# Kernel optimization log

Measured on AMD Instinct MI355X. Metric: run time of the kernel, lower is better.

Reference implementation:

```python
import jax, jax.numpy as jnp
import numpy as np

B, S, D = 4, 2048, 768
H = 12
DH = D // H
NUM_WAY = 4
DFF = 4 * D  # FFN expansion scale=4
EPS = 1e-6


def setup_inputs() -> dict:
    key = jax.random.key(0)
    ks = jax.random.split(key, 20)
    s = 0.02
    inp = {
        "x": jax.random.normal(ks[0], (B, S, D), jnp.float32),
        "w": jax.random.randint(ks[1], (B, S), 0, NUM_WAY, jnp.int64),
        # LayerNorm 1
        "ln1_g": jnp.ones((D,), jnp.float32),
        "ln1_b": jnp.zeros((D,), jnp.float32),
        # Multi-head attention projections (input_dim=out_dim=D)
        "wq": jax.random.normal(ks[2], (D, D), jnp.float32) * s,
        "bq": jnp.zeros((D,), jnp.float32),
        "wk": jax.random.normal(ks[3], (D, D), jnp.float32) * s,
        "bk": jnp.zeros((D,), jnp.float32),
        "wv": jax.random.normal(ks[4], (D, D), jnp.float32) * s,
        "bv": jnp.zeros((D,), jnp.float32),
        "wo": jax.random.normal(ks[5], (D, D), jnp.float32) * s,
        "bo": jnp.zeros((D,), jnp.float32),
        # Way classifier
        "wcls": jax.random.normal(ks[6], (D, NUM_WAY), jnp.float32) * s,
        "bcls": jnp.zeros((NUM_WAY,), jnp.float32),
        # num_way stacked FFN experts: Linear(D,4D) -> ReLU -> Linear(4D,D)
        "w1": jax.random.normal(ks[7], (NUM_WAY, D, DFF), jnp.float32) * s,
        "b1": jnp.zeros((NUM_WAY, DFF), jnp.float32),
        "w2": jax.random.normal(ks[8], (NUM_WAY, DFF, D), jnp.float32) * s,
        "b2": jnp.zeros((NUM_WAY, D), jnp.float32),
    }
    return inp


def _layernorm(x, g, b):
    mu = jnp.mean(x, axis=-1, keepdims=True)
    var = jnp.mean(jnp.square(x - mu), axis=-1, keepdims=True)
    return (x - mu) * jax.lax.rsqrt(var + EPS) * g + b


def reference(x, w, ln1_g, ln1_b, wq, bq, wk, bk, wv, bv, wo, bo,
              wcls, bcls, w1, b1, w2, b2):
    # pre-LN
    xn = _layernorm(x, ln1_g, ln1_b)
    # multi-head self-attention (q = k = v = xn)
    q = (xn @ wq + bq).reshape(B, S, H, DH)
    k = (xn @ wk + bk).reshape(B, S, H, DH)
    v = (xn @ wv + bv).reshape(B, S, H, DH)
    scores = jnp.einsum('bqhd,bkhd->bhqk', q, k) / jnp.sqrt(jnp.float32(DH))
    attn = jax.nn.softmax(scores, axis=-1)
    ctx = jnp.einsum('bhqk,bkhd->bqhd', attn, v).reshape(B, S, D)
    ctx = ctx @ wo + bo
    # dropout is identity at inference; residual
    out = ctx + x
    # dense compute-all-experts FFN, then per-token select by routing id w
    # (mask-overwrite in original == one-hot select since masks partition)
    ffn_out = jnp.zeros_like(out)
    for ci in range(NUM_WAY):
        h = jax.nn.relu(out @ w1[ci] + b1[ci])        # [B,S,4D]
        fi = h @ w2[ci] + b2[ci]                      # [B,S,D]
        mask = (w == ci).astype(out.dtype)[..., None]  # [B,S,1]
        if ci == 0:
            # original initializes ffn_out with way-0 output everywhere;
            # later ways overwrite where w == ci, net = select expert w
            ffn_out = fi
        else:
            ffn_out = ffn_out * (1.0 - mask) + fi * mask
    way_logits = out @ wcls + bcls  # [B,S,NUM_WAY]
    return ffn_out, way_logits
```

## Files before the change

### kernel.cpp

```cpp
#include <hip/hip_runtime.h>
#include <cstdint>

typedef unsigned short u16;
typedef float f32x4 __attribute__((ext_vector_type(4)));
typedef float f32x16 __attribute__((ext_vector_type(16)));
typedef __bf16 bf16x8 __attribute__((ext_vector_type(8)));

#define LOG2E 1.44269504088896340736f

__device__ __forceinline__ u16 f2bf(float f) {
    union { float f; unsigned u; } v; v.f = f;
    unsigned r = v.u + 0x7fffu + ((v.u >> 16) & 1u);
    return (u16)(r >> 16);
}

__device__ __forceinline__ unsigned cvt_pk_bf16(float lo, float hi) {
    unsigned r;
    asm("v_cvt_pk_bf16_f32 %0, %1, %2" : "=v"(r) : "v"(lo), "v"(hi));
    return r;
}

__device__ __forceinline__ float exp2_hw(float x) {
    float r;
    asm("v_exp_f32 %0, %1" : "=v"(r) : "v"(x));
    return r;
}

__device__ __forceinline__ f32x4 mfma16(bf16x8 a, bf16x8 b, f32x4 c) {
    return __builtin_amdgcn_mfma_f32_16x16x32_bf16(a, b, c, 0, 0, 0);
}

__device__ __forceinline__ f32x16 mfma32(bf16x8 a, bf16x8 b, f32x16 c) {
    return __builtin_amdgcn_mfma_f32_32x32x16_bf16(a, b, c, 0, 0, 0);
}

__device__ __forceinline__ void gload_lds16(const void* g, void* l) {
    __builtin_amdgcn_global_load_lds(
        (__attribute__((address_space(1))) unsigned int*)(g),
        (__attribute__((address_space(3))) unsigned int*)(l),
        16, 0, 0);
}

#define MB_TOK 8192
#define DM 768
#define HH 12
#define DHD 64
#define NWAY 4
#define DFF 3072
#define SEQ 2048
#define NBATCH 4

__global__ __launch_bounds__(256) void ln_kernel(
    const float* __restrict__ x, const float* __restrict__ g,
    const float* __restrict__ bb, u16* __restrict__ xn)
{
    int row = blockIdx.x, t = threadIdx.x;
    const float* xr = x + (size_t)row * DM;
    float v0 = xr[t], v1 = xr[t + 256], v2 = xr[t + 512];
    float s = v0 + v1 + v2;
    __shared__ float red[4];
    #pragma unroll
    for (int k = 1; k < 64; k <<= 1) s += __shfl_xor(s, k);
    if ((t & 63) == 0) red[t >> 6] = s;
    __syncthreads();
    float mu = (red[0] + red[1] + red[2] + red[3]) * (1.f / 768.f);
    float d0 = v0 - mu, d1 = v1 - mu, d2 = v2 - mu;
    float q = d0 * d0 + d1 * d1 + d2 * d2;
    #pragma unroll
    for (int k = 1; k < 64; k <<= 1) q += __shfl_xor(q, k);
    __syncthreads();
    if ((t & 63) == 0) red[t >> 6] = q;
    __syncthreads();
    float var = (red[0] + red[1] + red[2] + red[3]) * (1.f / 768.f);
    float rs = rsqrtf(var + 1e-6f);
    u16* xo = xn + (size_t)row * DM;
    xo[t]       = f2bf(d0 * rs * g[t]       + bb[t]);
    xo[t + 256] = f2bf(d1 * rs * g[t + 256] + bb[t + 256]);
    xo[t + 512] = f2bf(d2 * rs * g[t + 512] + bb[t + 512]);
}

__global__ __launch_bounds__(256) void transpose_bf16(
    const float* __restrict__ src, u16* __restrict__ dst, int K, int N)
{
    __shared__ float tl[32][33];
    size_t bofs = (size_t)blockIdx.z * K * N;
    src += bofs; dst += bofs;
    int n0 = blockIdx.x * 32, k0 = blockIdx.y * 32;
    int tx = threadIdx.x, ty = threadIdx.y;
    #pragma unroll
    for (int j = 0; j < 4; ++j)
        tl[ty + j * 8][tx] = src[(size_t)(k0 + ty + j * 8) * N + n0 + tx];
    __syncthreads();
    #pragma unroll
    for (int j = 0; j < 4; ++j)
        dst[(size_t)(n0 + ty + j * 8) * K + k0 + tx] = f2bf(tl[tx][ty + j * 8]);
}

__global__ __launch_bounds__(256) void vT_kernel(
    const u16* __restrict__ qkv, u16* __restrict__ vT)
{
    __shared__ u16 tl[32][33];
    int bh = blockIdx.z;
    int b = bh / HH, h = bh % HH;
    int key0 = blockIdx.x * 32;
    int d0 = blockIdx.y * 32;
    int tx = threadIdx.x, ty = threadIdx.y;
    const u16* src = qkv + ((size_t)b * SEQ + key0) * 2304 + 1536 + h * 64 + d0;
    #pragma unroll
    for (int j = 0; j < 4; ++j)
        tl[ty + j * 8][tx] = src[(size_t)(ty + j * 8) * 2304 + tx];
    __syncthreads();
    u16* dst = vT + ((size_t)bh * 64 + d0) * SEQ + key0;
    #pragma unroll
    for (int j = 0; j < 4; ++j)
        dst[(size_t)(ty + j * 8) * SEQ + tx] = tl[tx][ty + j * 8];
}

__global__ void concat_bias_kernel(const float* bq, const float* bk,
                                   const float* bv, float* bqkv)
{
    int i = blockIdx.x * 256 + threadIdx.x;
    if (i < 2304) bqkv[i] = i < 768 ? bq[i] : (i < 1536 ? bk[i - 768] : bv[i - 1536]);
}

__global__ void route_kernel(const int* __restrict__ wl,
                             int* __restrict__ perm, int* __restrict__ eoff,
                             int4* __restrict__ fmap)
{
    __shared__ int cnt[4], cur[4], off[5];
    int tid = threadIdx.x;
    if (tid < 4) cnt[tid] = 0;
    __syncthreads();
    for (int t = tid; t < MB_TOK; t += 256) atomicAdd(&cnt[wl[t] & 3], 1);
    __syncthreads();
    if (tid == 0) {
        off[0] = 0;
        for (int e = 0; e < 4; ++e) off[e + 1] = off[e] + cnt[e];
        int idx = 0;
        for (int e = 0; e < 4; ++e)
            for (int s = 0; s < cnt[e]; s += 128)
                fmap[idx++] = make_int4(e, off[e], s, cnt[e] - s);
        for (; idx < 72; ++idx) fmap[idx] = make_int4(-1, 0, 0, 0);
        for (int e = 0; e < 5; ++e) eoff[e] = off[e];
        for (int e = 0; e < 4; ++e) cur[e] = off[e];
    }
    __syncthreads();
    for (int t = tid; t < MB_TOK; t += 256) {
        int e = wl[t] & 3;
        int pos = atomicAdd(&cur[e], 1);
        perm[pos] = t;
    }
}

template<int MODE, bool RELU, bool RES, bool ST32, bool ST16>
__global__ __launch_bounds__(256, 3) void gemm_bt_kernel(
    const u16* __restrict__ A, const u16* __restrict__ Bt,
    const float* __restrict__ bias, const float* __restrict__ res,
    float* __restrict__ out32, u16* __restrict__ out16,
    int nbt, int N, int K, int ntn,
    const int* __restrict__ perm, const int4* __restrict__ fmap)
{
    __shared__ __attribute__((aligned(16))) u16 As[2][4096];
    __shared__ __attribute__((aligned(16))) u16 Bs[2][4096];
    int tid = threadIdx.x;
    int wv = tid >> 6, ln = tid & 63;
    int bpx = gridDim.x / (ntn << 3);
    int jj = blockIdx.x >> 3;
    int bt = (blockIdx.x & 7) * bpx + jj / ntn;
    int tn = (jj % ntn) * 128;
    if (bt >= nbt) return;

    int seg = 0, ms = 0, mb = 128, tm = 0;
    if (MODE != 0) {
        int4 ent = fmap[bt];
        if (ent.x < 0) return;
        seg = ent.y; ms = ent.z; mb = ent.w; if (mb > 128) mb = 128;
        Bt += (size_t)ent.x * N * K;
        bias += ent.x * N;
    } else {
        tm = bt * 128;
    }

    f32x4 acc[4][4];
    #pragma unroll
    for (int i = 0; i < 4; ++i)
        #pragma unroll
        for (int j = 0; j < 4; ++j) acc[i][j] = f32x4{0.f, 0.f, 0.f, 0.f};

    int wr = wv >> 1, wc = wv & 1;
    int lr = ln & 15, hi = ln >> 4;
    int nk = K / 32;

    const u16* asrc[2];
    const u16* bsrc[2];
    #pragma unroll
    for (int i = 0; i < 2; ++i) {
        int r = (wv * 2 + i) * 16 + (ln >> 2);
        int am = r < mb ? r : (mb - 1);
        size_t arow;
        if (MODE == 1)      arow = (size_t)perm[seg + ms + am];
        else if (MODE == 2) arow = (size_t)(seg + ms + am);
        else                arow = (size_t)(tm + r);
        asrc[i] = A + arow * K + (ln & 3) * 8;
        bsrc[i] = Bt + (size_t)(tn + r) * K + (ln & 3) * 8;
    }

#define GSTAGE(bf_, k0_) do {                                             \
    gload_lds16(asrc[0] + (k0_), &As[bf_][(wv * 2) * 512]);               \
    gload_lds16(asrc[1] + (k0_), &As[bf_][(wv * 2 + 1) * 512]);           \
    gload_lds16(bsrc[0] + (k0_), &Bs[bf_][(wv * 2) * 512]);               \
    gload_lds16(bsrc[1] + (k0_), &Bs[bf_][(wv * 2 + 1) * 512]);           \
} while (0)

    GSTAGE(0, 0);
    for (int kk = 0; kk < nk; ++kk) {
        int bf = kk & 1;
        __syncthreads();
        if (kk + 1 < nk) GSTAGE(bf ^ 1, (kk + 1) * 32);
        bf16x8 a[4], b[4];
        #pragma unroll
        for (int m = 0; m < 4; ++m)
            a[m] = *(const bf16x8*)&As[bf][(wr * 64 + m * 16 + lr) * 32 + hi * 8];
        #pragma unroll
        for (int n = 0; n < 4; ++n)
            b[n] = *(const bf16x8*)&Bs[bf][(wc * 64 + n * 16 + lr) * 32 + hi * 8];
        #pragma unroll
        for (int m = 0; m < 4; ++m)
            #pragma unroll
            for (int n = 0; n < 4; ++n)
                acc[m][n] = mfma16(a[m], b[n], acc[m][n]);
    }
#undef GSTAGE

    #pragma unroll
    for (int m = 0; m < 4; ++m) {
        int rb = wr * 64 + m * 16 + hi * 4;
        #pragma unroll
        for (int n = 0; n < 4; ++n) {
            int gcol = tn + wc * 64 + n * 16 + lr;
            float bvv = bias[gcol];
            #pragma unroll
            for (int i = 0; i < 4; ++i) {
                int rml = rb + i;
                float v = acc[m][n][i] + bvv;
                if (RELU) v = v > 0.f ? v : 0.f;
                if (MODE == 0) {
                    size_t grow = (size_t)(tm + rml);
                    if (RES) v += res[grow * N + gcol];
                    if (ST32) out32[grow * N + gcol] = v;
                    if (ST16) out16[grow * N + gcol] = f2bf(v);
                } else {
                    if (rml < mb) {
                        size_t orow = (MODE == 1) ? (size_t)(seg + ms + rml)
                                                  : (size_t)perm[seg + ms + rml];
                        if (ST32) out32[orow * N + gcol] = v;
                        if (ST16) out16[orow * N + gcol] = f2bf(v);
                    }
                }
            }
        }
    }
}

__global__ __launch_bounds__(256, 4) void attn_kernel(
    const u16* __restrict__ qkv, const u16* __restrict__ vT,
    u16* __restrict__ ctx)
{
    __shared__ __attribute__((aligned(16))) u16 Ks[2][4096];
    __shared__ __attribute__((aligned(16))) u16 Vs[2][4096];
    int tid = threadIdx.x;
    int wv = tid >> 6, ln = tid & 63;
    int qv = ln & 31, hi = ln >> 5;
    int bid = blockIdx.x;
    int bh = (bid & 7) * 6 + ((bid >> 3) % 6);
    int qt = (bid >> 3) / 6;
    int b = bh / HH, h = bh % HH;
    int q0 = qt * 128 + wv * 32;
    size_t qrowb = (size_t)(b * SEQ + q0);
    const float C = 0.125f * LOG2E;

    bf16x8 qf[4];
    {
        const u16* qp = qkv + (qrowb + qv) * 2304 + h * 64 + hi * 8;
        #pragma unroll
        for (int ds = 0; ds < 4; ++ds) qf[ds] = *(const bf16x8*)(qp + ds * 16);
    }

    int csrc = 8 * ((ln & 7) ^ (ln >> 3));
    const size_t kbase = (size_t)b * SEQ * 2304 + 768 + h * 64;
    const u16* vtb = vT + (size_t)bh * 64 * SEQ;
    const u16* kp0 = qkv + kbase + (size_t)(wv * 16 + (ln >> 3)) * 2304 + csrc;
    const u16* kp1 = kp0 + (size_t)8 * 2304;
    const u16* vp0 = vtb + (size_t)(wv * 16 + (ln >> 3)) * SEQ + csrc;
    const u16* vp1 = vp0 + (size_t)8 * SEQ;

#define ATTN_STAGE(bf_, t_) do {                                          \
    gload_lds16(kp0 + (size_t)(t_) * 64 * 2304, &Ks[bf_][(wv * 2) * 512]);\
    gload_lds16(kp1 + (size_t)(t_) * 64 * 2304, &Ks[bf_][(wv * 2 + 1) * 512]);\
    gload_lds16(vp0 + (size_t)(t_) * 64, &Vs[bf_][(wv * 2) * 512]);       \
    gload_lds16(vp1 + (size_t)(t_) * 64, &Vs[bf_][(wv * 2 + 1) * 512]);   \
} while (0)

    f32x16 oacc[2];
    #pragma unroll
    for (int i = 0; i < 2; ++i)
        #pragma unroll
        for (int r = 0; r < 16; ++r) oacc[i][r] = 0.f;
    float m_run = -INFINITY, l_run = 0.f;
    int ksw = (qv & 7) * 8;

    ATTN_STAGE(0, 0);

    for (int kt = 0; kt < SEQ / 64; ++kt) {
        int bf = kt & 1;
        __syncthreads();
        if (kt + 1 < SEQ / 64) ATTN_STAGE(bf ^ 1, kt + 1);

        f32x16 s0, s1;
        #pragma unroll
        for (int r = 0; r < 16; ++r) { s0[r] = 0.f; s1[r] = 0.f; }
        #pragma unroll
        for (int ds = 0; ds < 4; ++ds) {
            bf16x8 ka0 = *(const bf16x8*)&Ks[bf][qv * 64 + ((ds * 16 + hi * 8) ^ ksw)];
            bf16x8 ka1 = *(const bf16x8*)&Ks[bf][(32 + qv) * 64 + ((ds * 16 + hi * 8) ^ ksw)];
            s0 = mfma32(ka0, qf[ds], s0);
            s1 = mfma32(ka1, qf[ds], s1);
        }

        float tmax = s0[0];
        #pragma unroll
        for (int r = 1; r < 16; ++r) tmax = fmaxf(tmax, s0[r]);
        #pragma unroll
        for (int r = 0; r < 16; ++r) tmax = fmaxf(tmax, s1[r]);
        tmax = fmaxf(tmax, __shfl_xor(tmax, 32));

        if (!__all(tmax - m_run <= 64.f)) {
            float m_new = fmaxf(m_run, tmax);
            float corr = exp2_hw((m_run - m_new) * C);
            l_run *= corr;
            #pragma unroll
            for (int i = 0; i < 2; ++i)
                #pragma unroll
                for (int r = 0; r < 16; ++r) oacc[i][r] *= corr;
            m_run = m_new;
        }
        float c2 = -m_run * C;
        float psum = 0.f;
        #pragma unroll
        for (int r = 0; r < 16; ++r) {
            s0[r] = exp2_hw(fmaf(s0[r], C, c2)); psum += s0[r];
            s1[r] = exp2_hw(fmaf(s1[r], C, c2)); psum += s1[r];
        }
        l_run += psum;

        #pragma unroll
        for (int kb = 0; kb < 2; ++kb) {
            #pragma unroll
            for (int hc = 0; hc < 2; ++hc) {
                const f32x16& sv = kb ? s1 : s0;
                unsigned x0 = cvt_pk_bf16(sv[8 * hc + 0], sv[8 * hc + 1]);
                unsigned x1 = cvt_pk_bf16(sv[8 * hc + 2], sv[8 * hc + 3]);
                unsigned x2 = cvt_pk_bf16(sv[8 * hc + 4], sv[8 * hc + 5]);
                unsigned x3 = cvt_pk_bf16(sv[8 * hc + 6], sv[8 * hc + 7]);
                unsigned t0 = hi ? x0 : x2, t1 = hi ? x1 : x3;
                unsigned r0 = (unsigned)__shfl_xor((int)t0, 32);
                unsigned r1 = (unsigned)__shfl_xor((int)t1, 32);
                union { bf16x8 v; unsigned u[4]; } pf;
                pf.u[0] = hi ? r0 : x0; pf.u[1] = hi ? r1 : x1;
                pf.u[2] = hi ? x2 : r0; pf.u[3] = hi ? x3 : r1;
                int kc = (kb * 32 + hc * 16 + hi * 8) ^ ksw;
                #pragma unroll
                for (int dblk = 0; dblk < 2; ++dblk) {
                    bf16x8 va = *(const bf16x8*)&Vs[bf][(dblk * 32 + qv) * 64 + kc];
                    oacc[dblk] = mfma32(va, pf.v, oacc[dblk]);
                }
            }
        }
    }
#undef ATTN_STAGE

    float l_tot = l_run + __shfl_xor(l_run, 32);
    float inv = 1.f / l_tot;

    __syncthreads();
    u16* eb = &Ks[0][0] + wv * 2048;
    #pragma unroll
    for (int dblk = 0; dblk < 2; ++dblk)
        #pragma unroll
        for (int r = 0; r < 16; r += 2) {
            int d = dblk * 32 + (r & 3) + 8 * (r >> 2) + 4 * hi;
            unsigned pk = cvt_pk_bf16(oacc[dblk][r] * inv, oacc[dblk][r + 1] * inv);
            *(unsigned*)&eb[qv * 64 + (d ^ ((qv & 7) * 8))] = pk;
        }
    __syncthreads();
    {
        u16* ctr = ctx + (qrowb + qv) * DM + h * 64 + hi * 32;
        #pragma unroll
        for (int g = 0; g < 4; ++g) {
            bf16x8 vv = *(const bf16x8*)&eb[qv * 64 + ((hi * 32 + g * 8) ^ ((qv & 7) * 8))];
            *(bf16x8*)(ctr + g * 8) = vv;
        }
    }
}

__global__ __launch_bounds__(256) void cls_kernel(
    const float* __restrict__ outm, const float* __restrict__ wcls,
    const float* __restrict__ bcls, float* __restrict__ dst)
{
    int row = blockIdx.x, t = threadIdx.x;
    const float* xr = outm + (size_t)row * DM;
    float a0 = 0, a1 = 0, a2 = 0, a3 = 0;
    for (int j = t; j < DM; j += 256) {
        float xv = xr[j];
        float4 wv4 = *(const float4*)(const void*)(wcls + (size_t)j * 4);
        a0 += xv * wv4.x; a1 += xv * wv4.y; a2 += xv * wv4.z; a3 += xv * wv4.w;
    }
    #pragma unroll
    for (int k = 1; k < 64; k <<= 1) {
        a0 += __shfl_xor(a0, k); a1 += __shfl_xor(a1, k);
        a2 += __shfl_xor(a2, k); a3 += __shfl_xor(a3, k);
    }
    __shared__ float red[4][4];
    if ((t & 63) == 0) {
        int wid = t >> 6;
        red[wid][0] = a0; red[wid][1] = a1; red[wid][2] = a2; red[wid][3] = a3;
    }
    __syncthreads();
    if (t < 4)
        dst[(size_t)row * 4 + t] =
            red[0][t] + red[1][t] + red[2][t] + red[3][t] + bcls[t];
}

extern "C" void kernel_launch(void* const* d_in, const int* in_sizes, int n_in,
                              void* d_out, int out_size, void* d_ws, size_t ws_size,
                              hipStream_t stream) {
    const float* x      = (const float*)d_in[0];
    const int*   wl     = (const int*)d_in[1];
    const float* ln_g   = (const float*)d_in[2];
    const float* ln_b   = (const float*)d_in[3];
    const float* wq     = (const float*)d_in[4];
    const float* bq     = (const float*)d_in[5];
    const float* wk     = (const float*)d_in[6];
    const float* bk     = (const float*)d_in[7];
    const float* wvv    = (const float*)d_in[8];
    const float* bv     = (const float*)d_in[9];
    const float* wo     = (const float*)d_in[10];
    const float* bo     = (const float*)d_in[11];
    const float* wcls   = (const float*)d_in[12];
    const float* bcls   = (const float*)d_in[13];
    const float* w1     = (const float*)d_in[14];
    const float* b1     = (const float*)d_in[15];
    const float* w2     = (const float*)d_in[16];
    const float* b2     = (const float*)d_in[17];
    float* out = (float*)d_out;

    char* ws = (char*)d_ws;
    u16*   xn    = (u16*)  (ws + 0);
    u16*   qkv   = (u16*)  (ws + 12582912);
    u16*   hbuf  = (u16*)  (ws + 0);
    u16*   ctx   = (u16*)  (ws + 50331648);
    u16*   outb  = (u16*)  (ws + 62914560);
    u16*   wqkvt = (u16*)  (ws + 75497472);
    u16*   wot   = (u16*)  (ws + 79036416);
    u16*   w1t   = (u16*)  (ws + 80216064);
    u16*   w2t   = (u16*)  (ws + 99090432);
    float* bqkv  = (float*)(ws + 117964800);
    int*   perm  = (int*)  (ws + 117974016);
    int*   eoff  = (int*)  (ws + 118006784);
    int4*  fmap  = (int4*) (ws + 118006816);
    u16*   vT    = (u16*)  (ws + 118007968);
    float* outf  = out;

    route_kernel<<<1, 256, 0, stream>>>(wl, perm, eoff, fmap);
    concat_bias_kernel<<<9, 256, 0, stream>>>(bq, bk, bv, bqkv);
    dim3 tb(32, 8);
    transpose_bf16<<<dim3(24, 24, 1), tb, 0, stream>>>(wq,  wqkvt,             768, 768);
    transpose_bf16<<<dim3(24, 24, 1), tb, 0, stream>>>(wk,  wqkvt + 768 * 768, 768, 768);
    transpose_bf16<<<dim3(24, 24, 1), tb, 0, stream>>>(wvv, wqkvt + 2 * 768 * 768, 768, 768);
    transpose_bf16<<<dim3(24, 24, 1), tb, 0, stream>>>(wo,  wot, 768, 768);
    transpose_bf16<<<dim3(96, 24, 4), tb, 0, stream>>>(w1,  w1t, 768, 3072);
    transpose_bf16<<<dim3(24, 96, 4), tb, 0, stream>>>(w2,  w2t, 3072, 768);
    ln_kernel<<<MB_TOK, 256, 0, stream>>>(x, ln_g, ln_b, xn);

    gemm_bt_kernel<0, false, false, false, true><<<1152, 256, 0, stream>>>(
        xn, wqkvt, bqkv, nullptr, nullptr, qkv, 64, 2304, 768, 18, nullptr, nullptr);

    vT_kernel<<<dim3(64, 2, 48), tb, 0, stream>>>(qkv, vT);

    attn_kernel<<<768, 256, 0, stream>>>(qkv, vT, ctx);

    gemm_bt_kernel<0, false, true, true, true><<<384, 256, 0, stream>>>(
        ctx, wot, bo, x, outf, outb, 64, 768, 768, 6, nullptr, nullptr);

    cls_kernel<<<MB_TOK, 256, 0, stream>>>(outf, wcls, bcls, out + (size_t)MB_TOK * DM);

    gemm_bt_kernel<1, true, false, false, true><<<1728, 256, 0, stream>>>(
        outb, w1t, b1, nullptr, nullptr, hbuf, 72, DFF, 768, 24, perm, fmap);

    gemm_bt_kernel<2, false, false, true, false><<<432, 256, 0, stream>>>(
        hbuf, w2t, b2, nullptr, out, nullptr, 72, 768, DFF, 6, perm, fmap);
}
```

Baseline: 373.1 us.

## Triple-buffer GEMM loads and use 64-row tiles for narrow-N GEMMs

The GEMM kernel moves from a double-buffered to a triple-buffered LDS pipeline, waiting on vmcnt with a barrier so two stages stay in flight. It also gains a TM=64 variant with a 64x128 tile and four waves each covering 32 columns. The output projection and the second FFN GEMM (N=768) use this variant to launch more blocks and get better CU occupancy, and the router emits a second 64-row segment map for the FFN2 GEMM. The costs are more LDS per block and less reuse per tile in the 64-row variant.

```diff
diff --git a/kernel.cpp b/kernel.cpp
--- a/kernel.cpp
+++ b/kernel.cpp
@@ -125,7 +125,7 @@
 
 __global__ void route_kernel(const int* __restrict__ wl,
                              int* __restrict__ perm, int* __restrict__ eoff,
-                             int4* __restrict__ fmap)
+                             int4* __restrict__ fmap, int4* __restrict__ fmap64)
 {
     __shared__ int cnt[4], cur[4], off[5];
     int tid = threadIdx.x;
@@ -141,6 +141,11 @@
             for (int s = 0; s < cnt[e]; s += 128)
                 fmap[idx++] = make_int4(e, off[e], s, cnt[e] - s);
         for (; idx < 72; ++idx) fmap[idx] = make_int4(-1, 0, 0, 0);
+        int idx2 = 0;
+        for (int e = 0; e < 4; ++e)
+            for (int s = 0; s < cnt[e]; s += 64)
+                fmap64[idx2++] = make_int4(e, off[e], s, cnt[e] - s);
+        for (; idx2 < 136; ++idx2) fmap64[idx2] = make_int4(-1, 0, 0, 0);
         for (int e = 0; e < 5; ++e) eoff[e] = off[e];
         for (int e = 0; e < 4; ++e) cur[e] = off[e];
     }
@@ -152,16 +157,20 @@
     }
 }
 
-template<int MODE, bool RELU, bool RES, bool ST32, bool ST16>
-__global__ __launch_bounds__(256, 3) void gemm_bt_kernel(
+template<int MODE, int TM, bool RELU, bool RES, bool ST32, bool ST16>
+__global__ __launch_bounds__(256, (TM == 64) ? 4 : 3) void gemm_bt_kernel(
     const u16* __restrict__ A, const u16* __restrict__ Bt,
     const float* __restrict__ bias, const float* __restrict__ res,
     float* __restrict__ out32, u16* __restrict__ out16,
     int nbt, int N, int K, int ntn,
     const int* __restrict__ perm, const int4* __restrict__ fmap)
 {
-    __shared__ __attribute__((aligned(16))) u16 As[2][4096];
-    __shared__ __attribute__((aligned(16))) u16 Bs[2][4096];
+    constexpr int ALD = TM * 32;
+    constexpr int BLD = 128 * 32;
+    constexpr int NLD = (TM == 128) ? 4 : 3;
+    constexpr int NN  = (TM == 64) ? 2 : 4;
+    __shared__ __attribute__((aligned(16))) u16 As[3][ALD];
+    __shared__ __attribute__((aligned(16))) u16 Bs[3][BLD];
     int tid = threadIdx.x;
     int wv = tid >> 6, ln = tid & 63;
     int bpx = gridDim.x / (ntn << 3);
@@ -170,24 +179,25 @@
     int tn = (jj % ntn) * 128;
     if (bt >= nbt) return;
 
-    int seg = 0, ms = 0, mb = 128, tm = 0;
+    int seg = 0, ms = 0, mb = TM, tm = 0;
     if (MODE != 0) {
         int4 ent = fmap[bt];
         if (ent.x < 0) return;
-        seg = ent.y; ms = ent.z; mb = ent.w; if (mb > 128) mb = 128;
+        seg = ent.y; ms = ent.z; mb = ent.w; if (mb > TM) mb = TM;
         Bt += (size_t)ent.x * N * K;
         bias += ent.x * N;
     } else {
-        tm = bt * 128;
-    }
-
-    f32x4 acc[4][4];
+        tm = bt * TM;
+    }
+
+    f32x4 acc[4][NN];
     #pragma unroll
     for (int i = 0; i < 4; ++i)
         #pragma unroll
-        for (int j = 0; j < 4; ++j) acc[i][j] = f32x4{0.f, 0.f, 0.f, 0.f};
-
-    int wr = wv >> 1, wc = wv & 1;
+        for (int j = 0; j < NN; ++j) acc[i][j] = f32x4{0.f, 0.f, 0.f, 0.f};
+
+    int wr = (TM == 128) ? (wv >> 1) : 0;
+    int wcol0 = (TM == 128) ? (wv & 1) * 64 : wv * 32;
     int lr = ln & 15, hi = ln >> 4;
     int nk = K / 32;
 
@@ -195,40 +205,60 @@
     const u16* bsrc[2];
     #pragma unroll
     for (int i = 0; i < 2; ++i) {
-        int r = (wv * 2 + i) * 16 + (ln >> 2);
-        int am = r < mb ? r : (mb - 1);
-        size_t arow;
-        if (MODE == 1)      arow = (size_t)perm[seg + ms + am];
-        else if (MODE == 2) arow = (size_t)(seg + ms + am);
-        else                arow = (size_t)(tm + r);
-        asrc[i] = A + arow * K + (ln & 3) * 8;
-        bsrc[i] = Bt + (size_t)(tn + r) * K + (ln & 3) * 8;
-    }
-
-#define GSTAGE(bf_, k0_) do {                                             \
-    gload_lds16(asrc[0] + (k0_), &As[bf_][(wv * 2) * 512]);               \
-    gload_lds16(asrc[1] + (k0_), &As[bf_][(wv * 2 + 1) * 512]);           \
-    gload_lds16(bsrc[0] + (k0_), &Bs[bf_][(wv * 2) * 512]);               \
-    gload_lds16(bsrc[1] + (k0_), &Bs[bf_][(wv * 2 + 1) * 512]);           \
+        int rb2 = (TM == 128) ? ((wv * 2 + i) * 16 + (ln >> 2))
+                              : (wv * 16 + (ln >> 2));
+        if (TM == 128 || i == 0) {
+            int am = rb2 < mb ? rb2 : (mb - 1);
+            size_t arow;
+            if (MODE == 1)      arow = (size_t)perm[seg + ms + am];
+            else if (MODE == 2) arow = (size_t)(seg + ms + am);
+            else                arow = (size_t)(tm + rb2);
+            asrc[i] = A + arow * K + (ln & 3) * 8;
+        }
+        int rB = (wv * 2 + i) * 16 + (ln >> 2);
+        bsrc[i] = Bt + (size_t)(tn + rB) * K + (ln & 3) * 8;
+    }
+    int aofs0 = (TM == 128) ? (wv * 2) * 512 : wv * 512;
+    int bofs0 = (wv * 2) * 512, bofs1 = (wv * 2 + 1) * 512;
+
+#define GSTAGE(ab_, bb_, k0_) do {                                        \
+    gload_lds16(asrc[0] + (k0_), (ab_) + aofs0);                          \
+    if (TM == 128) gload_lds16(asrc[1] + (k0_), (ab_) + aofs0 + 512);     \
+    gload_lds16(bsrc[0] + (k0_), (bb_) + bofs0);                          \
+    gload_lds16(bsrc[1] + (k0_), (bb_) + bofs1);                          \
 } while (0)
 
-    GSTAGE(0, 0);
+    u16* A0 = &As[0][0];
+    u16* B0 = &Bs[0][0];
+    GSTAGE(A0, B0, 0);
+    GSTAGE(A0 + ALD, B0 + BLD, 32);
+    int bf3 = 0;
     for (int kk = 0; kk < nk; ++kk) {
-        int bf = kk & 1;
-        __syncthreads();
-        if (kk + 1 < nk) GSTAGE(bf ^ 1, (kk + 1) * 32);
-        bf16x8 a[4], b[4];
+        if (kk + 1 < nk)
+            asm volatile("s_waitcnt vmcnt(%0) lgkmcnt(0)" :: "i"(NLD) : "memory");
+        else
+            asm volatile("s_waitcnt vmcnt(0) lgkmcnt(0)" ::: "memory");
+        __builtin_amdgcn_s_barrier();
+        __builtin_amdgcn_sched_barrier(0);
+        if (kk + 2 < nk) {
+            int nb = bf3 + 2; if (nb >= 3) nb -= 3;
+            GSTAGE(A0 + nb * ALD, B0 + nb * BLD, (kk + 2) * 32);
+        }
+        const u16* Ab = A0 + bf3 * ALD;
+        const u16* Bb = B0 + bf3 * BLD;
+        bf16x8 a[4], b[NN];
         #pragma unroll
         for (int m = 0; m < 4; ++m)
-            a[m] = *(const bf16x8*)&As[bf][(wr * 64 + m * 16 + lr) * 32 + hi * 8];
-        #pragma unroll
-        for (int n = 0; n < 4; ++n)
-            b[n] = *(const bf16x8*)&Bs[bf][(wc * 64 + n * 16 + lr) * 32 + hi * 8];
+            a[m] = *(const bf16x8*)&Ab[(wr * 64 + m * 16 + lr) * 32 + hi * 8];
+        #pragma unroll
+        for (int n = 0; n < NN; ++n)
+            b[n] = *(const bf16x8*)&Bb[(wcol0 + n * 16 + lr) * 32 + hi * 8];
         #pragma unroll
         for (int m = 0; m < 4; ++m)
             #pragma unroll
-            for (int n = 0; n < 4; ++n)
+            for (int n = 0; n < NN; ++n)
                 acc[m][n] = mfma16(a[m], b[n], acc[m][n]);
+        bf3 = (bf3 == 2) ? 0 : bf3 + 1;
     }
 #undef GSTAGE
 
@@ -236,8 +266,8 @@
     for (int m = 0; m < 4; ++m) {
         int rb = wr * 64 + m * 16 + hi * 4;
         #pragma unroll
-        for (int n = 0; n < 4; ++n) {
-            int gcol = tn + wc * 64 + n * 16 + lr;
+        for (int n = 0; n < NN; ++n) {
+            int gcol = tn + wcol0 + n * 16 + lr;
             float bvv = bias[gcol];
             #pragma unroll
             for (int i = 0; i < 4; ++i) {
@@ -468,10 +498,11 @@
     int*   perm  = (int*)  (ws + 117974016);
     int*   eoff  = (int*)  (ws + 118006784);
     int4*  fmap  = (int4*) (ws + 118006816);
-    u16*   vT    = (u16*)  (ws + 118007968);
+    int4*  fmap64= (int4*) (ws + 118007968);
+    u16*   vT    = (u16*)  (ws + 118010144);
     float* outf  = out;
 
-    route_kernel<<<1, 256, 0, stream>>>(wl, perm, eoff, fmap);
+    route_kernel<<<1, 256, 0, stream>>>(wl, perm, eoff, fmap, fmap64);
     concat_bias_kernel<<<9, 256, 0, stream>>>(bq, bk, bv, bqkv);
     dim3 tb(32, 8);
     transpose_bf16<<<dim3(24, 24, 1), tb, 0, stream>>>(wq,  wqkvt,             768, 768);
@@ -482,21 +513,21 @@
     transpose_bf16<<<dim3(24, 96, 4), tb, 0, stream>>>(w2,  w2t, 3072, 768);
     ln_kernel<<<MB_TOK, 256, 0, stream>>>(x, ln_g, ln_b, xn);
 
-    gemm_bt_kernel<0, false, false, false, true><<<1152, 256, 0, stream>>>(
+    gemm_bt_kernel<0, 128, false, false, false, true><<<1152, 256, 0, stream>>>(
         xn, wqkvt, bqkv, nullptr, nullptr, qkv, 64, 2304, 768, 18, nullptr, nullptr);
 
     vT_kernel<<<dim3(64, 2, 48), tb, 0, stream>>>(qkv, vT);
 
     attn_kernel<<<768, 256, 0, stream>>>(qkv, vT, ctx);
 
-    gemm_bt_kernel<0, false, true, true, true><<<384, 256, 0, stream>>>(
-        ctx, wot, bo, x, outf, outb, 64, 768, 768, 6, nullptr, nullptr);
+    gemm_bt_kernel<0, 64, false, true, true, true><<<768, 256, 0, stream>>>(
+        ctx, wot, bo, x, outf, outb, 128, 768, 768, 6, nullptr, nullptr);
 
     cls_kernel<<<MB_TOK, 256, 0, stream>>>(outf, wcls, bcls, out + (size_t)MB_TOK * DM);
 
-    gemm_bt_kernel<1, true, false, false, true><<<1728, 256, 0, stream>>>(
+    gemm_bt_kernel<1, 128, true, false, false, true><<<1728, 256, 0, stream>>>(
         outb, w1t, b1, nullptr, nullptr, hbuf, 72, DFF, 768, 24, perm, fmap);
 
-    gemm_bt_kernel<2, false, false, true, false><<<432, 256, 0, stream>>>(
-        hbuf, w2t, b2, nullptr, out, nullptr, 72, 768, DFF, 6, perm, fmap);
-}
+    gemm_bt_kernel<2, 64, false, false, true, false><<<816, 256, 0, stream>>>(
+        hbuf, w2t, b2, nullptr, out, nullptr, 136, 768, DFF, 6, perm, fmap64);
+}
```

Measured after the change: 395.7 us. 1.06x slower.
